# Performance work log

Measured on AMD Instinct MI355X. Metric: run time of the kernel, lower is better.

## Reference

```python
import jax, jax.numpy as jnp
import numpy as np

B, S, H = 1, 2048, 4608
NH, NKV, HD = 36, 4, 128
GROUP = NH // NKV  # 9
ROPE_THETA = 100000.0
SLIDING_WINDOW = 1024


def _rope_tables(seq_len, head_dim):
    inv_freq = 1.0 / (ROPE_THETA ** (jnp.arange(0, head_dim, 2, dtype=jnp.float32) / head_dim))
    ang = jnp.arange(seq_len, dtype=jnp.float32)[:, None] * inv_freq[None, :]  # [S, HD/2]
    emb = jnp.concatenate([ang, ang], axis=-1)  # [S, HD]
    return jnp.cos(emb), jnp.sin(emb)


def setup_inputs() -> dict:
    key = jax.random.key(0)
    ks = jax.random.split(key, 10)
    std = 0.02
    cos_table, sin_table = _rope_tables(S, HD)
    return {
        "hidden_states": jax.random.normal(ks[0], (B, S, H), jnp.float32),
        "position_ids": jnp.broadcast_to(jnp.arange(S, dtype=jnp.int64)[None, :], (B, S)),
        "cos_table": cos_table,
        "sin_table": sin_table,
        "q_w": jax.random.normal(ks[1], (NH * HD, H), jnp.float32) * std,
        "q_b": jax.random.normal(ks[2], (NH * HD,), jnp.float32) * std,
        "k_w": jax.random.normal(ks[3], (NKV * HD, H), jnp.float32) * std,
        "k_b": jax.random.normal(ks[4], (NKV * HD,), jnp.float32) * std,
        "v_w": jax.random.normal(ks[5], (NKV * HD, H), jnp.float32) * std,
        "v_b": jax.random.normal(ks[6], (NKV * HD,), jnp.float32) * std,
        "o_w": jax.random.normal(ks[7], (H, NH * HD), jnp.float32) * std,
        "o_b": jax.random.normal(ks[8], (H,), jnp.float32) * std,
        "sliding_window": SLIDING_WINDOW,
    }


def _rotate_half(x):
    x1, x2 = jnp.split(x, 2, axis=-1)
    return jnp.concatenate([-x2, x1], axis=-1)


def reference(hidden_states, position_ids, cos_table, sin_table,
              q_w, q_b, k_w, k_b, v_w, v_b, o_w, o_b, sliding_window):
    bsz, q_len, _ = hidden_states.shape
    scaling = HD ** -0.5

    q = (hidden_states @ q_w.T + q_b).reshape(bsz, q_len, NH, HD)
    k = (hidden_states @ k_w.T + k_b).reshape(bsz, q_len, NKV, HD)
    v = (hidden_states @ v_w.T + v_b).reshape(bsz, q_len, NKV, HD)

    # RoPE with explicit cos/sin, unsqueeze_dim=2 ('bsnd' layout)
    cos = cos_table[position_ids][:, :, None, :]  # [B, S, 1, HD]
    sin = sin_table[position_ids][:, :, None, :]
    q = q * cos + _rotate_half(q) * sin
    k = k * cos + _rotate_half(k) * sin

    # GQA: group Q heads per KV head
    qg = q.reshape(bsz, q_len, NKV, GROUP, HD)
    logits = jnp.einsum('bqgrd,bkgd->bgrqk', qg, k) * scaling  # [B, NKV, GROUP, S, S]

    # causal + sliding-window mask: attend where k <= q and q - k < window
    idx = jnp.arange(q_len)
    mask = (idx[:, None] >= idx[None, :]) & (idx[:, None] - idx[None, :] < sliding_window)
    logits = jnp.where(mask[None, None, None, :, :], logits, jnp.finfo(logits.dtype).min)

    probs = jax.nn.softmax(logits, axis=-1)
    attn = jnp.einsum('bgrqk,bkgd->bqgrd', probs, v).reshape(bsz, q_len, NH * HD)
    return attn @ o_w.T + o_b
```

## Files before the change

kernel.cpp:

```cpp
#include <hip/hip_runtime.h>
#include <stdint.h>

typedef __attribute__((ext_vector_type(8))) __bf16 bf16x8;
typedef __attribute__((ext_vector_type(4))) float f32x4;
typedef __attribute__((ext_vector_type(8))) unsigned short u16x8;
typedef __attribute__((ext_vector_type(4))) unsigned short u16x4;

#define SEQ 2048
#define HID 4608
#define NQKV 5632
#define NHEAD 36
#define NKVH 4
#define HDIM 128
#define WINDOW 1024

__device__ __forceinline__ unsigned short f2b(float f) {
    unsigned u = __builtin_bit_cast(unsigned, f);
    u += 0x7fffu + ((u >> 16) & 1u);
    return (unsigned short)(u >> 16);
}
__device__ __forceinline__ float b2f(unsigned short h) {
    unsigned u = ((unsigned)h) << 16;
    return __builtin_bit_cast(float, u);
}

#define GLD16(gp, lp) __builtin_amdgcn_global_load_lds( \
    (const __attribute__((address_space(1))) void*)(gp), \
    (__attribute__((address_space(3))) void*)(lp), 16, 0, 0)

#define VMCNT5() asm volatile("s_waitcnt vmcnt(5)" ::: "memory")
#define VMCNT4() asm volatile("s_waitcnt vmcnt(4)" ::: "memory")
#define VMCNT0() asm volatile("s_waitcnt vmcnt(0)" ::: "memory")
#define BARRIER() asm volatile("s_barrier" ::: "memory")

__global__ __launch_bounds__(256) void conv_all_kernel(
    const float* __restrict__ s0, unsigned short* __restrict__ d0, int n0,
    const float* __restrict__ s1, unsigned short* __restrict__ d1, int n1,
    const float* __restrict__ s2, unsigned short* __restrict__ d2, int n2,
    const float* __restrict__ s3, unsigned short* __restrict__ d3, int n3)
{
    int total = n0 + n1 + n2 + n3;
    int stride = gridDim.x * blockDim.x;
    for (int i = blockIdx.x * blockDim.x + threadIdx.x; i < total; i += stride) {
        const float* src; unsigned short* dst; int j = i;
        if (j < n0) { src = s0; dst = d0; }
        else if ((j -= n0) < n1) { src = s1; dst = d1; }
        else if ((j -= n1) < n2) { src = s2; dst = d2; }
        else { j -= n2; src = s3; dst = d3; }
        float4 v = ((const float4*)src)[j];
        ushort4 o;
        o.x = f2b(v.x); o.y = f2b(v.y); o.z = f2b(v.z); o.w = f2b(v.w);
        ((ushort4*)dst)[j] = o;
    }
}

__global__ __launch_bounds__(512, 4) void gemm_qkv_kernel(
    const unsigned short* __restrict__ A,
    const unsigned short* __restrict__ W,
    unsigned short* __restrict__ out,
    const float* __restrict__ b0, const float* __restrict__ b1, const float* __restrict__ b2,
    int N, int K, int GX, int GB,
    const float* __restrict__ cw_src, unsigned short* __restrict__ cw_dst, int cw_n4)
{
    const int tid = threadIdx.x;
    const int o = blockIdx.x;

    if (o >= GB) {
        int cb = o - GB, ncb = gridDim.x - GB;
        int stride = ncb * 512;
        for (int i = cb * 512 + tid; i < cw_n4; i += stride) {
            float4 v = ((const float4*)cw_src)[i];
            ushort4 u;
            u.x = f2b(v.x); u.y = f2b(v.y); u.z = f2b(v.z); u.w = f2b(v.w);
            ((ushort4*)cw_dst)[i] = u;
        }
        return;
    }

    __shared__ alignas(16) unsigned short ldsA[2][128 * 64];
    __shared__ alignas(16) unsigned short ldsB[2][128 * 64];

    const int w = tid >> 6, lane = tid & 63;
    const int r16 = lane & 15, kg = lane >> 4;
    const int wm = w >> 2, wn = w & 3;

    const int cpx = GB >> 3;
    const int id = (o & 7) * cpx + (o >> 3);
    const int bx = id % GX, by = id / GX;
    const int row0 = by * 128, col0 = bx * 128;

    const int lr = lane >> 3;
    const int lc = lane & 7;
    const int cg = lc ^ lr;
    const unsigned short* Abase = A + (size_t)row0 * K;
    const unsigned short* Wbase = W + (size_t)col0 * K;

    auto STG = [&](const unsigned short* Mat, unsigned short* slot, int kb) {
#pragma unroll
        for (int j = 0; j < 2; ++j) {
            int row = (w * 2 + j) * 8 + lr;
            GLD16(Mat + (size_t)row * K + kb + cg * 8,
                  (char*)slot + (w * 2 + j) * 1024);
        }
    };

    const int NITER = K >> 7;
    f32x4 acc[4][2] = {};
    const int swz = r16 & 7;

    bf16x8 af[4][2], bf[2][2];

#define DSR_AF(Sl) \
_Pragma("unroll") for (int mi = 0; mi < 4; ++mi) \
_Pragma("unroll") for (int kh = 0; kh < 2; ++kh) \
    af[mi][kh] = *(const bf16x8*)((Sl) + (wm * 64 + mi * 16 + r16) * 64 + ((kh * 4 + kg) ^ swz) * 8);
#define DSR_BF(Sl) \
_Pragma("unroll") for (int ni = 0; ni < 2; ++ni) \
_Pragma("unroll") for (int kh = 0; kh < 2; ++kh) \
    bf[ni][kh] = *(const bf16x8*)((Sl) + (wn * 32 + ni * 16 + r16) * 64 + ((kh * 4 + kg) ^ swz) * 8);
#define MFMA8(half) \
    asm volatile("s_waitcnt lgkmcnt(0)" ::: "memory"); \
    __builtin_amdgcn_sched_barrier(0); \
    __builtin_amdgcn_s_setprio(1); \
_Pragma("unroll") for (int mi = 0; mi < 2; ++mi) \
_Pragma("unroll") for (int ni = 0; ni < 2; ++ni) \
_Pragma("unroll") for (int kh = 0; kh < 2; ++kh) \
    acc[(half) * 2 + mi][ni] = __builtin_amdgcn_mfma_f32_16x16x32_bf16(af[(half) * 2 + mi][kh], bf[ni][kh], acc[(half) * 2 + mi][ni], 0, 0, 0); \
    __builtin_amdgcn_s_setprio(0); \
    __builtin_amdgcn_sched_barrier(0);

    STG(Abase, ldsA[0], 0);  STG(Wbase, ldsB[0], 0);
    STG(Abase, ldsA[1], 64); STG(Wbase, ldsB[1], 64);
    VMCNT0();
    BARRIER();

    for (int i = 0; i < NITER; ++i) {
        const bool st = (i + 1 < NITER);
        const int kb0 = (i + 1) * 128;
        const int kb1 = kb0 + 64;

        DSR_AF(ldsA[0]); DSR_BF(ldsB[0]);
        BARRIER();
        MFMA8(0);
        BARRIER();
        if (st) { STG(Abase, ldsA[0], kb0); STG(Wbase, ldsB[0], kb0); VMCNT4(); } else { VMCNT0(); }
        BARRIER();
        MFMA8(1);
        BARRIER();
        DSR_AF(ldsA[1]); DSR_BF(ldsB[1]);
        BARRIER();
        MFMA8(0);
        BARRIER();
        if (st) { STG(Abase, ldsA[1], kb1); STG(Wbase, ldsB[1], kb1); VMCNT4(); }
        BARRIER();
        MFMA8(1);
        BARRIER();
    }

#pragma unroll
    for (int m = 0; m < 4; ++m)
#pragma unroll
        for (int n = 0; n < 2; ++n)
#pragma unroll
            for (int r = 0; r < 4; ++r) {
                int row = row0 + wm * 64 + m * 16 + kg * 4 + r;
                int col = col0 + wn * 32 + n * 16 + r16;
                float bias = (col < HID) ? b0[col]
                           : (col < HID + 512 ? b1[col - HID] : b2[col - HID - 512]);
                out[(size_t)row * N + col] = f2b(acc[m][n][r] + bias);
            }
#undef DSR_AF
#undef DSR_BF
#undef MFMA8
}

__global__ __launch_bounds__(512, 4) void gemm_op_kernel(
    const unsigned short* __restrict__ A,
    const unsigned short* __restrict__ W,
    float* __restrict__ out,
    const float* __restrict__ b0,
    int N, int K, int GX)
{
    __shared__ alignas(16) unsigned short ldsA[2][128 * 64];
    __shared__ alignas(16) unsigned short ldsB[2][192 * 64];

    const int tid = threadIdx.x;
    const int w = tid >> 6, lane = tid & 63;
    const int r16 = lane & 15, kg = lane >> 4;
    const int wm = w >> 2, wn = w & 3;

    const int cpx = gridDim.x >> 3;
    const int o = blockIdx.x;
    const int id = (o & 7) * cpx + (o >> 3);
    const int bx = id % GX, by = id / GX;
    const int row0 = by * 128, col0 = bx * 192;

    const int lr = lane >> 3;
    const int lc = lane & 7;
    const int cg = lc ^ lr;
    const unsigned short* Abase = A + (size_t)row0 * K;
    const unsigned short* Wbase = W + (size_t)col0 * K;

    auto STGA = [&](unsigned short* slot, int kb) {
#pragma unroll
        for (int j = 0; j < 2; ++j) {
            int row = (w * 2 + j) * 8 + lr;
            GLD16(Abase + (size_t)row * K + kb + cg * 8,
                  (char*)slot + (w * 2 + j) * 1024);
        }
    };
    auto STGB = [&](unsigned short* slot, int kb) {
#pragma unroll
        for (int j3 = 0; j3 < 3; ++j3) {
            int row = j3 * 64 + w * 8 + lr;
            GLD16(Wbase + (size_t)row * K + kb + cg * 8,
                  (char*)slot + j3 * 8192 + w * 1024);
        }
    };

    const int NITER = K >> 7;
    f32x4 acc[4][3] = {};
    const int swz = r16 & 7;

    bf16x8 af[4][2], bf[3][2];

#define DSR_AF(Sl) \
_Pragma("unroll") for (int mi = 0; mi < 4; ++mi) \
_Pragma("unroll") for (int kh = 0; kh < 2; ++kh) \
    af[mi][kh] = *(const bf16x8*)((Sl) + (wm * 64 + mi * 16 + r16) * 64 + ((kh * 4 + kg) ^ swz) * 8);
#define DSR_BF(Sl) \
_Pragma("unroll") for (int ni = 0; ni < 3; ++ni) \
_Pragma("unroll") for (int kh = 0; kh < 2; ++kh) \
    bf[ni][kh] = *(const bf16x8*)((Sl) + (wn * 48 + ni * 16 + r16) * 64 + ((kh * 4 + kg) ^ swz) * 8);
#define MFMA12(half) \
    asm volatile("s_waitcnt lgkmcnt(0)" ::: "memory"); \
    __builtin_amdgcn_sched_barrier(0); \
    __builtin_amdgcn_s_setprio(1); \
_Pragma("unroll") for (int mi = 0; mi < 2; ++mi) \
_Pragma("unroll") for (int ni = 0; ni < 3; ++ni) \
_Pragma("unroll") for (int kh = 0; kh < 2; ++kh) \
    acc[(half) * 2 + mi][ni] = __builtin_amdgcn_mfma_f32_16x16x32_bf16(af[(half) * 2 + mi][kh], bf[ni][kh], acc[(half) * 2 + mi][ni], 0, 0, 0); \
    __builtin_amdgcn_s_setprio(0); \
    __builtin_amdgcn_sched_barrier(0);

    STGA(ldsA[0], 0);  STGB(ldsB[0], 0);
    STGA(ldsA[1], 64); STGB(ldsB[1], 64);
    VMCNT0();
    BARRIER();

    for (int i = 0; i < NITER; ++i) {
        const bool st = (i + 1 < NITER);
        const int kb0 = (i + 1) * 128;
        const int kb1 = kb0 + 64;

        DSR_AF(ldsA[0]); DSR_BF(ldsB[0]);
        BARRIER();
        MFMA12(0);
        BARRIER();
        if (st) { STGA(ldsA[0], kb0); STGB(ldsB[0], kb0); VMCNT5(); } else { VMCNT0(); }
        BARRIER();
        MFMA12(1);
        BARRIER();
        DSR_AF(ldsA[1]); DSR_BF(ldsB[1]);
        BARRIER();
        MFMA12(0);
        BARRIER();
        if (st) { STGA(ldsA[1], kb1); STGB(ldsB[1], kb1); VMCNT5(); }
        BARRIER();
        MFMA12(1);
        BARRIER();
    }

#pragma unroll
    for (int m = 0; m < 4; ++m)
#pragma unroll
        for (int n = 0; n < 3; ++n)
#pragma unroll
            for (int r = 0; r < 4; ++r) {
                int row = row0 + wm * 64 + m * 16 + kg * 4 + r;
                int col = col0 + wn * 48 + n * 16 + r16;
                out[(size_t)row * N + col] = acc[m][n][r] + b0[col];
            }
#undef DSR_AF
#undef DSR_BF
#undef MFMA12
}

__global__ __launch_bounds__(256) void rope_vt_kernel(unsigned short* __restrict__ qkv,
                                                      const float* __restrict__ cos_t,
                                                      const float* __restrict__ sin_t,
                                                      unsigned short* __restrict__ vtg) {
    const int bid = blockIdx.x;
    if (bid < 5120) {
        int idx = bid * 256 + threadIdx.x;
        int d4 = idx & 15;
        int t2 = idx >> 4;
        int head = t2 % 40;
        int s = t2 / 40;
        int base = head < NHEAD ? head * HDIM : HID + (head - NHEAD) * HDIM;
        size_t off = (size_t)s * NQKV + base + d4 * 4;
        u16x4 xv = *(const u16x4*)(qkv + off);
        u16x4 yv = *(const u16x4*)(qkv + off + 64);
        float4 c = *(const float4*)(cos_t + s * HDIM + d4 * 4);
        float4 sn = *(const float4*)(sin_t + s * HDIM + d4 * 4);
        u16x4 xo, yo;
        float x, y;
        x = b2f(xv[0]); y = b2f(yv[0]); xo[0] = f2b(x * c.x - y * sn.x); yo[0] = f2b(y * c.x + x * sn.x);
        x = b2f(xv[1]); y = b2f(yv[1]); xo[1] = f2b(x * c.y - y * sn.y); yo[1] = f2b(y * c.y + x * sn.y);
        x = b2f(xv[2]); y = b2f(yv[2]); xo[2] = f2b(x * c.z - y * sn.z); yo[2] = f2b(y * c.z + x * sn.z);
        x = b2f(xv[3]); y = b2f(yv[3]); xo[3] = f2b(x * c.w - y * sn.w); yo[3] = f2b(y * c.w + x * sn.w);
        *(u16x4*)(qkv + off) = xo;
        *(u16x4*)(qkv + off + 64) = yo;
    } else {
        __shared__ unsigned short tile[32][36];
        int vb = bid - 5120;
        const int s0 = (vb & 63) * 32;
        const int d0 = ((vb >> 6) & 3) * 32;
        const int kvh = vb >> 8;
        const int lid = threadIdx.x;
        {
            int sl = lid >> 3, dc = (lid & 7) * 4;
            u16x4 v = *(const u16x4*)(qkv + (size_t)(s0 + sl) * NQKV + HID + 512 + kvh * HDIM + d0 + dc);
#pragma unroll
            for (int i = 0; i < 4; ++i) tile[sl][dc + i] = v[i];
        }
        __syncthreads();
        {
            int dl = lid >> 3, sc = (lid & 7) * 4;
            u16x4 v;
#pragma unroll
            for (int i = 0; i < 4; ++i) v[i] = tile[sc + i][dl];
            *(u16x4*)(vtg + (size_t)kvh * HDIM * SEQ + (size_t)(d0 + dl) * SEQ + s0 + sc) = v;
        }
    }
}

#define KSTR 136
#define VSTR 72
#define PSTR 88
__global__ __launch_bounds__(256) void attn_kernel(const unsigned short* __restrict__ qkv,
                                                   const unsigned short* __restrict__ vtg,
                                                   unsigned short* __restrict__ aout)
{
    __shared__ alignas(16) unsigned short Ks[64 * KSTR];
    __shared__ alignas(16) unsigned short Vt[128 * VSTR];
    __shared__ alignas(16) unsigned short Ps[4 * 16 * PSTR];
    const int h = blockIdx.x, qb = blockIdx.y;
    const int q0 = qb * 64;
    const int kvh = h / 9;
    const int tid = threadIdx.x, wid = tid >> 6, lane = tid & 63;
    const int r16 = lane & 15, kg = lane >> 4;
    const int qbase = q0 + wid * 16;
    const unsigned short* vsrc = vtg + (size_t)kvh * HDIM * SEQ;

    bf16x8 qf[4];
    {
        const unsigned short* qrow = qkv + (size_t)(qbase + r16) * NQKV + h * HDIM;
#pragma unroll
        for (int kk = 0; kk < 4; ++kk)
            qf[kk] = *(const bf16x8*)(qrow + kk * 32 + kg * 8);
    }

    f32x4 o[8] = {};
    float mrow[4], lrow[4];
#pragma unroll
    for (int r = 0; r < 4; ++r) { mrow[r] = -1e30f; lrow[r] = 0.f; }

    int lo = q0 - (WINDOW - 1); if (lo < 0) lo = 0; lo &= ~63;
    unsigned short* myP = Ps + wid * 16 * PSTR;
    const float scale = 0.08838834764831845f;

    u16x8 kreg[4], vreg[4];
#define PREF(KT) \
_Pragma("unroll") for (int j = 0; j < 4; ++j) { \
        int c = tid + j * 256; \
        int key = c >> 4, dc = c & 15; \
        kreg[j] = *(const u16x8*)(qkv + (size_t)((KT) + key) * NQKV + HID + kvh * HDIM + dc * 8); \
        int d = c >> 3, k8 = (c & 7) * 8; \
        vreg[j] = *(const u16x8*)(vsrc + (size_t)d * SEQ + (KT) + k8); \
    }

    PREF(lo);

    for (int kt = lo; kt <= q0; kt += 64) {
#pragma unroll
        for (int j = 0; j < 4; ++j) {
            int c = tid + j * 256;
            int key = c >> 4, dc = c & 15;
            *(u16x8*)(Ks + key * KSTR + dc * 8) = kreg[j];
            int d = c >> 3, k8 = (c & 7) * 8;
            *(u16x8*)(Vt + d * VSTR + k8) = vreg[j];
        }
        __syncthreads();

        if (kt + 64 <= q0) { PREF(kt + 64); }

        f32x4 sc[4] = {};
#pragma unroll
        for (int t = 0; t < 4; ++t)
#pragma unroll
            for (int kk = 0; kk < 4; ++kk) {
                bf16x8 kf = *(const bf16x8*)(Ks + (t * 16 + r16) * KSTR + kk * 32 + kg * 8);
                sc[t] = __builtin_amdgcn_mfma_f32_16x16x32_bf16(qf[kk], kf, sc[t], 0, 0, 0);
            }

        float p[4][4], mt[4];
#pragma unroll
        for (int r = 0; r < 4; ++r) mt[r] = -1e30f;
        const bool fullv = (kt + 63 <= qbase) && (qbase + 15 - kt < WINDOW);
        if (fullv) {
#pragma unroll
            for (int t = 0; t < 4; ++t)
#pragma unroll
                for (int r = 0; r < 4; ++r) {
                    float v = sc[t][r] * scale;
                    p[t][r] = v;
                    mt[r] = fmaxf(mt[r], v);
                }
        } else {
#pragma unroll
            for (int t = 0; t < 4; ++t)
#pragma unroll
                for (int r = 0; r < 4; ++r) {
                    int q = qbase + kg * 4 + r;
                    int key = kt + t * 16 + r16;
                    bool valid = (key <= q) && (q - key < WINDOW);
                    float v = valid ? sc[t][r] * scale : -1e30f;
                    p[t][r] = v;
                    mt[r] = fmaxf(mt[r], v);
                }
        }
#pragma unroll
        for (int mask = 1; mask <= 8; mask <<= 1)
#pragma unroll
            for (int r = 0; r < 4; ++r)
                mt[r] = fmaxf(mt[r], __shfl_xor(mt[r], mask, 64));

        float alpha[4], tsum[4];
#pragma unroll
        for (int r = 0; r < 4; ++r) {
            float mnew = fmaxf(mrow[r], mt[r]);
            alpha[r] = __expf(mrow[r] - mnew);
            mrow[r] = mnew;
            tsum[r] = 0.f;
        }
#pragma unroll
        for (int t = 0; t < 4; ++t)
#pragma unroll
            for (int r = 0; r < 4; ++r) {
                float e = __expf(p[t][r] - mrow[r]);
                p[t][r] = e;
                tsum[r] += e;
            }
#pragma unroll
        for (int mask = 1; mask <= 8; mask <<= 1)
#pragma unroll
            for (int r = 0; r < 4; ++r)
                tsum[r] += __shfl_xor(tsum[r], mask, 64);
#pragma unroll
        for (int r = 0; r < 4; ++r)
            lrow[r] = lrow[r] * alpha[r] + tsum[r];
#pragma unroll
        for (int n = 0; n < 8; ++n)
#pragma unroll
            for (int r = 0; r < 4; ++r)
                o[n][r] = o[n][r] * alpha[r];

#pragma unroll
        for (int t = 0; t < 4; ++t)
#pragma unroll
            for (int r = 0; r < 4; ++r)
                myP[(kg * 4 + r) * PSTR + t * 16 + r16] = f2b(p[t][r]);
        asm volatile("s_waitcnt lgkmcnt(0)" ::: "memory");

#pragma unroll
        for (int kc = 0; kc < 2; ++kc) {
            bf16x8 pa = *(const bf16x8*)(myP + r16 * PSTR + kc * 32 + kg * 8);
#pragma unroll
            for (int n = 0; n < 8; ++n) {
                bf16x8 vb = *(const bf16x8*)(Vt + (n * 16 + r16) * VSTR + kc * 32 + kg * 8);
                o[n] = __builtin_amdgcn_mfma_f32_16x16x32_bf16(pa, vb, o[n], 0, 0, 0);
            }
        }
        BARRIER();
    }
#undef PREF

#pragma unroll
    for (int n = 0; n < 8; ++n)
#pragma unroll
        for (int r = 0; r < 4; ++r) {
            int q = qbase + kg * 4 + r;
            aout[(size_t)q * HID + h * HDIM + n * 16 + r16] = f2b(o[n][r] / lrow[r]);
        }
}

extern "C" void kernel_launch(void* const* d_in, const int* in_sizes, int n_in,
                              void* d_out, int out_size, void* d_ws, size_t ws_size,
                              hipStream_t stream) {
    const float* hidden = (const float*)d_in[0];
    const float* cos_t = (const float*)d_in[2];
    const float* sin_t = (const float*)d_in[3];
    const float* q_w = (const float*)d_in[4];
    const float* q_b = (const float*)d_in[5];
    const float* k_w = (const float*)d_in[6];
    const float* k_b = (const float*)d_in[7];
    const float* v_w = (const float*)d_in[8];
    const float* v_b = (const float*)d_in[9];
    const float* o_w = (const float*)d_in[10];
    const float* o_b = (const float*)d_in[11];

    char* ws = (char*)d_ws;
    unsigned short* hbf  = (unsigned short*)ws;
    unsigned short* attn = hbf;
    unsigned short* wqkv = (unsigned short*)(ws + 18874368);
    unsigned short* vtg  = wqkv;
    unsigned short* wo   = (unsigned short*)(ws + 70778880);
    unsigned short* qkv  = (unsigned short*)(ws + 113246208);

    dim3 blk(256);
    conv_all_kernel<<<4096, blk, 0, stream>>>(
        hidden, hbf,                          (SEQ * HID) / 4,
        q_w,    wqkv,                         (HID * HID) / 4,
        k_w,    wqkv + (size_t)HID * HID,     (512 * HID) / 4,
        v_w,    wqkv + (size_t)5120 * HID,    (512 * HID) / 4);

    gemm_qkv_kernel<<<dim3(832), dim3(512), 0, stream>>>(
        hbf, wqkv, qkv, q_b, k_b, v_b, NQKV, HID, 44, 704,
        o_w, wo, (HID * HID) / 4);
    rope_vt_kernel<<<6144, blk, 0, stream>>>(qkv, cos_t, sin_t, vtg);
    attn_kernel<<<dim3(NHEAD, SEQ / 64), blk, 0, stream>>>(qkv, vtg, attn);
    gemm_op_kernel<<<dim3(384), dim3(512), 0, stream>>>(
        attn, wo, (float*)d_out, o_b, HID, HID, 24);
}
```

Baseline: 381.7 us.

## Widen QKV GEMM tile to 128x192 and move o_w conversion into attention launch

The QKV projection GEMM now uses 128x192 output tiles (3 N-subtiles per wave) over 480 blocks instead of 128x128 tiles over 704 blocks. The last column tile is clamped to overlap the previous one, which makes 5632 columns fit 30 tiles at the cost of recomputing some columns. The o_w fp32-to-bf16 conversion, previously done by extra blocks appended to the QKV GEMM grid, is now done by 128 extra blocks appended to a flattened 1D attention grid. The aim is more operand reuse per block and better wave quantization on the large GEMM, while hiding the weight conversion behind attention. The trade-off is higher register and LDS pressure in the GEMM.

```diff
diff --git a/kernel.cpp b/kernel.cpp
--- a/kernel.cpp
+++ b/kernel.cpp
@@ -29,7 +29,6 @@
     (__attribute__((address_space(3))) void*)(lp), 16, 0, 0)
 
 #define VMCNT5() asm volatile("s_waitcnt vmcnt(5)" ::: "memory")
-#define VMCNT4() asm volatile("s_waitcnt vmcnt(4)" ::: "memory")
 #define VMCNT0() asm volatile("s_waitcnt vmcnt(0)" ::: "memory")
 #define BARRIER() asm volatile("s_barrier" ::: "memory")
 
@@ -54,40 +53,27 @@
     }
 }
 
-__global__ __launch_bounds__(512, 4) void gemm_qkv_kernel(
+__global__ __launch_bounds__(512, 4) void gemm_qkv192_kernel(
     const unsigned short* __restrict__ A,
     const unsigned short* __restrict__ W,
     unsigned short* __restrict__ out,
     const float* __restrict__ b0, const float* __restrict__ b1, const float* __restrict__ b2,
-    int N, int K, int GX, int GB,
-    const float* __restrict__ cw_src, unsigned short* __restrict__ cw_dst, int cw_n4)
+    int N, int K, int GX)
 {
+    __shared__ alignas(16) unsigned short ldsA[2][128 * 64];
+    __shared__ alignas(16) unsigned short ldsB[2][192 * 64];
+
     const int tid = threadIdx.x;
-    const int o = blockIdx.x;
-
-    if (o >= GB) {
-        int cb = o - GB, ncb = gridDim.x - GB;
-        int stride = ncb * 512;
-        for (int i = cb * 512 + tid; i < cw_n4; i += stride) {
-            float4 v = ((const float4*)cw_src)[i];
-            ushort4 u;
-            u.x = f2b(v.x); u.y = f2b(v.y); u.z = f2b(v.z); u.w = f2b(v.w);
-            ((ushort4*)cw_dst)[i] = u;
-        }
-        return;
-    }
-
-    __shared__ alignas(16) unsigned short ldsA[2][128 * 64];
-    __shared__ alignas(16) unsigned short ldsB[2][128 * 64];
-
     const int w = tid >> 6, lane = tid & 63;
     const int r16 = lane & 15, kg = lane >> 4;
     const int wm = w >> 2, wn = w & 3;
 
-    const int cpx = GB >> 3;
+    const int cpx = gridDim.x >> 3;
+    const int o = blockIdx.x;
     const int id = (o & 7) * cpx + (o >> 3);
     const int bx = id % GX, by = id / GX;
-    const int row0 = by * 128, col0 = bx * 128;
+    const int row0 = by * 128;
+    int col0 = bx * 192; if (col0 + 192 > N) col0 = N - 192;
 
     const int lr = lane >> 3;
     const int lc = lane & 7;
@@ -95,42 +81,50 @@
     const unsigned short* Abase = A + (size_t)row0 * K;
     const unsigned short* Wbase = W + (size_t)col0 * K;
 
-    auto STG = [&](const unsigned short* Mat, unsigned short* slot, int kb) {
+    auto STGA = [&](unsigned short* slot, int kb) {
 #pragma unroll
         for (int j = 0; j < 2; ++j) {
             int row = (w * 2 + j) * 8 + lr;
-            GLD16(Mat + (size_t)row * K + kb + cg * 8,
+            GLD16(Abase + (size_t)row * K + kb + cg * 8,
                   (char*)slot + (w * 2 + j) * 1024);
         }
     };
+    auto STGB = [&](unsigned short* slot, int kb) {
+#pragma unroll
+        for (int j3 = 0; j3 < 3; ++j3) {
+            int row = j3 * 64 + w * 8 + lr;
+            GLD16(Wbase + (size_t)row * K + kb + cg * 8,
+                  (char*)slot + j3 * 8192 + w * 1024);
+        }
+    };
 
     const int NITER = K >> 7;
-    f32x4 acc[4][2] = {};
+    f32x4 acc[4][3] = {};
     const int swz = r16 & 7;
 
-    bf16x8 af[4][2], bf[2][2];
+    bf16x8 af[4][2], bf[3][2];
 
 #define DSR_AF(Sl) \
 _Pragma("unroll") for (int mi = 0; mi < 4; ++mi) \
 _Pragma("unroll") for (int kh = 0; kh < 2; ++kh) \
     af[mi][kh] = *(const bf16x8*)((Sl) + (wm * 64 + mi * 16 + r16) * 64 + ((kh * 4 + kg) ^ swz) * 8);
 #define DSR_BF(Sl) \
-_Pragma("unroll") for (int ni = 0; ni < 2; ++ni) \
+_Pragma("unroll") for (int ni = 0; ni < 3; ++ni) \
 _Pragma("unroll") for (int kh = 0; kh < 2; ++kh) \
-    bf[ni][kh] = *(const bf16x8*)((Sl) + (wn * 32 + ni * 16 + r16) * 64 + ((kh * 4 + kg) ^ swz) * 8);
-#define MFMA8(half) \
+    bf[ni][kh] = *(const bf16x8*)((Sl) + (wn * 48 + ni * 16 + r16) * 64 + ((kh * 4 + kg) ^ swz) * 8);
+#define MFMA12(half) \
     asm volatile("s_waitcnt lgkmcnt(0)" ::: "memory"); \
     __builtin_amdgcn_sched_barrier(0); \
     __builtin_amdgcn_s_setprio(1); \
 _Pragma("unroll") for (int mi = 0; mi < 2; ++mi) \
-_Pragma("unroll") for (int ni = 0; ni < 2; ++ni) \
+_Pragma("unroll") for (int ni = 0; ni < 3; ++ni) \
 _Pragma("unroll") for (int kh = 0; kh < 2; ++kh) \
     acc[(half) * 2 + mi][ni] = __builtin_amdgcn_mfma_f32_16x16x32_bf16(af[(half) * 2 + mi][kh], bf[ni][kh], acc[(half) * 2 + mi][ni], 0, 0, 0); \
     __builtin_amdgcn_s_setprio(0); \
     __builtin_amdgcn_sched_barrier(0);
 
-    STG(Abase, ldsA[0], 0);  STG(Wbase, ldsB[0], 0);
-    STG(Abase, ldsA[1], 64); STG(Wbase, ldsB[1], 64);
+    STGA(ldsA[0], 0);  STGB(ldsB[0], 0);
+    STGA(ldsA[1], 64); STGB(ldsB[1], 64);
     VMCNT0();
     BARRIER();
 
@@ -141,37 +135,37 @@
 
         DSR_AF(ldsA[0]); DSR_BF(ldsB[0]);
         BARRIER();
-        MFMA8(0);
-        BARRIER();
-        if (st) { STG(Abase, ldsA[0], kb0); STG(Wbase, ldsB[0], kb0); VMCNT4(); } else { VMCNT0(); }
-        BARRIER();
-        MFMA8(1);
+        MFMA12(0);
+        BARRIER();
+        if (st) { STGA(ldsA[0], kb0); STGB(ldsB[0], kb0); VMCNT5(); } else { VMCNT0(); }
+        BARRIER();
+        MFMA12(1);
         BARRIER();
         DSR_AF(ldsA[1]); DSR_BF(ldsB[1]);
         BARRIER();
-        MFMA8(0);
-        BARRIER();
-        if (st) { STG(Abase, ldsA[1], kb1); STG(Wbase, ldsB[1], kb1); VMCNT4(); }
-        BARRIER();
-        MFMA8(1);
+        MFMA12(0);
+        BARRIER();
+        if (st) { STGA(ldsA[1], kb1); STGB(ldsB[1], kb1); VMCNT5(); }
+        BARRIER();
+        MFMA12(1);
         BARRIER();
     }
 
 #pragma unroll
     for (int m = 0; m < 4; ++m)
 #pragma unroll
-        for (int n = 0; n < 2; ++n)
+        for (int n = 0; n < 3; ++n)
 #pragma unroll
             for (int r = 0; r < 4; ++r) {
                 int row = row0 + wm * 64 + m * 16 + kg * 4 + r;
-                int col = col0 + wn * 32 + n * 16 + r16;
+                int col = col0 + wn * 48 + n * 16 + r16;
                 float bias = (col < HID) ? b0[col]
                            : (col < HID + 512 ? b1[col - HID] : b2[col - HID - 512]);
                 out[(size_t)row * N + col] = f2b(acc[m][n][r] + bias);
             }
 #undef DSR_AF
 #undef DSR_BF
-#undef MFMA8
+#undef MFMA12
 }
 
 __global__ __launch_bounds__(512, 4) void gemm_op_kernel(
@@ -338,17 +332,35 @@
 #define KSTR 136
 #define VSTR 72
 #define PSTR 88
+#define NATT (NHEAD * (SEQ / 64))
 __global__ __launch_bounds__(256) void attn_kernel(const unsigned short* __restrict__ qkv,
                                                    const unsigned short* __restrict__ vtg,
-                                                   unsigned short* __restrict__ aout)
+                                                   unsigned short* __restrict__ aout,
+                                                   const float* __restrict__ cw_src,
+                                                   unsigned short* __restrict__ cw_dst, int cw_n4)
 {
     __shared__ alignas(16) unsigned short Ks[64 * KSTR];
     __shared__ alignas(16) unsigned short Vt[128 * VSTR];
     __shared__ alignas(16) unsigned short Ps[4 * 16 * PSTR];
-    const int h = blockIdx.x, qb = blockIdx.y;
+    const int bid = blockIdx.x;
+    const int tid = threadIdx.x;
+
+    if (bid >= NATT) {
+        int cb = bid - NATT, ncb = gridDim.x - NATT;
+        int stride = ncb * 256;
+        for (int i = cb * 256 + tid; i < cw_n4; i += stride) {
+            float4 v = ((const float4*)cw_src)[i];
+            ushort4 u;
+            u.x = f2b(v.x); u.y = f2b(v.y); u.z = f2b(v.z); u.w = f2b(v.w);
+            ((ushort4*)cw_dst)[i] = u;
+        }
+        return;
+    }
+
+    const int h = bid % NHEAD, qb = bid / NHEAD;
     const int q0 = qb * 64;
     const int kvh = h / 9;
-    const int tid = threadIdx.x, wid = tid >> 6, lane = tid & 63;
+    const int wid = tid >> 6, lane = tid & 63;
     const int r16 = lane & 15, kg = lane >> 4;
     const int qbase = q0 + wid * 16;
     const unsigned short* vsrc = vtg + (size_t)kvh * HDIM * SEQ;
@@ -525,11 +537,11 @@
         k_w,    wqkv + (size_t)HID * HID,     (512 * HID) / 4,
         v_w,    wqkv + (size_t)5120 * HID,    (512 * HID) / 4);
 
-    gemm_qkv_kernel<<<dim3(832), dim3(512), 0, stream>>>(
-        hbf, wqkv, qkv, q_b, k_b, v_b, NQKV, HID, 44, 704,
-        o_w, wo, (HID * HID) / 4);
+    gemm_qkv192_kernel<<<dim3(480), dim3(512), 0, stream>>>(
+        hbf, wqkv, qkv, q_b, k_b, v_b, NQKV, HID, 30);
     rope_vt_kernel<<<6144, blk, 0, stream>>>(qkv, cos_t, sin_t, vtg);
-    attn_kernel<<<dim3(NHEAD, SEQ / 64), blk, 0, stream>>>(qkv, vtg, attn);
+    attn_kernel<<<dim3(NATT + 128), blk, 0, stream>>>(
+        qkv, vtg, attn, o_w, wo, (HID * HID) / 4);
     gemm_op_kernel<<<dim3(384), dim3(512), 0, stream>>>(
         attn, wo, (float*)d_out, o_b, HID, HID, 24);
 }
```

Result: no change. 381.7 us (+0.0%).
